# Kernel tuning notes

Measured on AMD Instinct MI355X. Metric: run time of the kernel, lower is better.

## Reference

```python
import jax, jax.numpy as jnp
import numpy as np

NUM_HEADS = 16
KEY_DIM = 64
B, S, D = 2, 2048, 1024


def setup_inputs() -> dict:
    key = jax.random.key(0)
    ks = jax.random.split(key, 5)
    scale = 1.0 / np.sqrt(D)
    return {
        "x": jax.random.normal(ks[0], (B, S, D), dtype=jnp.float32),
        "Wq": jax.random.normal(ks[1], (D, NUM_HEADS * KEY_DIM), dtype=jnp.float32) * scale,
        "Wk": jax.random.normal(ks[2], (D, NUM_HEADS * KEY_DIM), dtype=jnp.float32) * scale,
        "Wv": jax.random.normal(ks[3], (D, NUM_HEADS * KEY_DIM), dtype=jnp.float32) * scale,
        "Wo": jax.random.normal(ks[4], (NUM_HEADS * KEY_DIM, D), dtype=jnp.float32) * scale,
    }


def reference(x, Wq, Wk, Wv, Wo):
    b, s, d = x.shape
    h, kd = NUM_HEADS, KEY_DIM
    # QKV projections -> [B, H, S, Kd]
    q = (x @ Wq).reshape(b, s, h, kd).transpose(0, 2, 1, 3)
    k = (x @ Wk).reshape(b, s, h, kd).transpose(0, 2, 1, 3)
    v = (x @ Wv).reshape(b, s, h, kd).transpose(0, 2, 1, 3)
    # scaled dot-product attention, full [B,H,S,S] scores (faithful to source)
    logits = jnp.einsum("bhqd,bhkd->bhqk", q, k) / jnp.sqrt(jnp.float32(kd))
    attn = jax.nn.softmax(logits, axis=-1)
    out = jnp.einsum("bhqk,bhkd->bhqd", attn, v)  # [B,H,S,Kd]
    out = out.transpose(0, 2, 1, 3).reshape(b, s, h * kd)
    return out @ Wo
```

## Files before the change

### kernel.cpp

```cpp
#include <hip/hip_runtime.h>


typedef __attribute__((ext_vector_type(8))) short short8;
typedef __attribute__((ext_vector_type(4))) float f32x4;

#define M_ROWS 4096
#define N_COLS 1024
#define K_DIM  1024
#define SEQ    2048

#define QSCALE 0.18033688011111772f

#if defined(__has_builtin)
#if __has_builtin(__builtin_amdgcn_exp2f)
#define EXP2(x) __builtin_amdgcn_exp2f(x)
#endif
#endif
#ifndef EXP2
#define EXP2(x) exp2f(x)
#endif

#define WAITCNT_VM8 0x0F78
#define WAITCNT_VM4 0x0F74

__device__ inline unsigned short f2bf(float f) {
  unsigned int u = __float_as_uint(f);
  u += 0x7fffu + ((u >> 16) & 1u);
  return (unsigned short)(u >> 16);
}

__device__ inline unsigned int pack2bf(float a, float b) {
  unsigned int ua = __float_as_uint(a); ua += 0x7fffu + ((ua >> 16) & 1u);
  unsigned int ub = __float_as_uint(b); ub += 0x7fffu + ((ub >> 16) & 1u);
  return (ua >> 16) | (ub & 0xffff0000u);
}

__device__ inline unsigned int cvtpk(float lo, float hi) {
  unsigned int r;
  asm("v_cvt_pk_bf16_f32 %0, %1, %2" : "=v"(r) : "v"(lo), "v"(hi));
  return r;
}

__device__ inline void swap32(unsigned int& a, unsigned int& b) {
  asm volatile("v_permlane32_swap_b32 %0, %1" : "+v"(a), "+v"(b));
}
__device__ inline void swap16(unsigned int& a, unsigned int& b) {
  asm volatile("v_permlane16_swap_b32 %0, %1" : "+v"(a), "+v"(b));
}

__device__ inline void async_load16(const unsigned short* gptr, unsigned short* lptr) {
  __builtin_amdgcn_global_load_lds(
      (const __attribute__((address_space(1))) unsigned int*)gptr,
      (__attribute__((address_space(3))) unsigned int*)lptr, 16, 0, 0);
}

__global__ void detect_kernel(const unsigned short* __restrict__ x, int* __restrict__ flag) {
  __shared__ int bad;
  if (threadIdx.x == 0) bad = 0;
  __syncthreads();
  for (int i = threadIdx.x; i < 1024; i += 256) {
    float f = __uint_as_float((unsigned int)x[i] << 16);
    float a = fabsf(f);
    if (!(a < 1e4f)) atomicOr(&bad, 1);
  }
  __syncthreads();
  if (threadIdx.x == 0) *flag = bad ? 0 : 1;
}

__global__ void convert_kernel(const void* __restrict__ src, unsigned short* __restrict__ dst,
                               int n4, const int* __restrict__ flag) {
  const int isbf = *flag;
  const int stride = gridDim.x * blockDim.x;
  for (int i = blockIdx.x * blockDim.x + threadIdx.x; i < n4; i += stride) {
    if (isbf) {
      ((uint2*)dst)[i] = ((const uint2*)src)[i];
    } else {
      float4 v = ((const float4*)src)[i];
      ushort4 o;
      o.x = f2bf(v.x); o.y = f2bf(v.y); o.z = f2bf(v.z); o.w = f2bf(v.w);
      ((ushort4*)dst)[i] = o;
    }
  }
}

__global__ __launch_bounds__(256) void convert_wT4_kernel(
    const void* __restrict__ s0, const void* __restrict__ s1,
    const void* __restrict__ s2, const void* __restrict__ s3,
    unsigned short* __restrict__ d0, unsigned short* __restrict__ d1,
    unsigned short* __restrict__ d2, unsigned short* __restrict__ d3,
    const int* __restrict__ flag) {
  __shared__ unsigned short t[32][33];
  const int z = blockIdx.z;
  const void* src = (z == 0) ? s0 : (z == 1) ? s1 : (z == 2) ? s2 : s3;
  unsigned short* dst = (z == 0) ? d0 : (z == 1) ? d1 : (z == 2) ? d2 : d3;
  const int tid = threadIdx.x;
  const int r0 = blockIdx.y * 32, c0 = blockIdx.x * 32;
  const int kr = tid >> 3, nc = (tid & 7) * 4;
  if (*flag) {
    const unsigned short* W = (const unsigned short*)src;
    uint2 v = *(const uint2*)(W + (size_t)(r0 + kr) * K_DIM + c0 + nc);
    t[kr][nc] = v.x & 0xffff; t[kr][nc + 1] = v.x >> 16;
    t[kr][nc + 2] = v.y & 0xffff; t[kr][nc + 3] = v.y >> 16;
  } else {
    const float* W = (const float*)src;
    float4 v = *(const float4*)(W + (size_t)(r0 + kr) * K_DIM + c0 + nc);
    t[kr][nc] = f2bf(v.x); t[kr][nc + 1] = f2bf(v.y);
    t[kr][nc + 2] = f2bf(v.z); t[kr][nc + 3] = f2bf(v.w);
  }
  __syncthreads();
  const int nr = tid >> 3, kc = (tid & 7) * 4;
  uint2 w;
  w.x = (unsigned int)t[kc][nr] | ((unsigned int)t[kc + 1][nr] << 16);
  w.y = (unsigned int)t[kc + 2][nr] | ((unsigned int)t[kc + 3][nr] << 16);
  *(uint2*)(dst + (size_t)(c0 + nr) * K_DIM + r0 + kc) = w;
}

#define GEMM_DMA(Aptr, Bptr, KTOT, KB, BUF)                                       \
  _Pragma("unroll") for (int r = 0; r < 2; ++r) {                                 \
    int s = r * 256 + wave * 64 + lane;                                           \
    int row = s >> 2, c = s & 3;                                                  \
    int g = c ^ ((row ^ (row >> 2)) & 3);                                         \
    async_load16((Aptr) + (size_t)(m0 + row) * (KTOT) + (KB) + g * 8,             \
                 &As[BUF][(size_t)(r * 256 + wave * 64) * 8]);                    \
    async_load16((Bptr) + (size_t)(n0 + row) * (KTOT) + (KB) + g * 8,             \
                 &Bs[BUF][(size_t)(r * 256 + wave * 64) * 8]);                    \
  }

#define GEMM_MAIN_LOOP(Aptr, Bptr, KTOT)                                          \
  f32x4 acc[4][4];                                                                \
  _Pragma("unroll") for (int i = 0; i < 4; ++i)                                   \
  _Pragma("unroll") for (int j = 0; j < 4; ++j)                                   \
      acc[i][j] = (f32x4){0.f, 0.f, 0.f, 0.f};                                    \
  const int xr = (l15 ^ (l15 >> 2)) & 3;                                          \
  GEMM_DMA(Aptr, Bptr, KTOT, 0, 0)                                                \
  for (int kb = 0; kb < (KTOT); kb += 32) {                                       \
    const int pp = (kb >> 5) & 1;                                                 \
    const int kbn = (kb + 32) & ((KTOT) - 1);                                     \
    GEMM_DMA(Aptr, Bptr, KTOT, kbn, pp ^ 1)                                       \
    __builtin_amdgcn_s_waitcnt(WAITCNT_VM4);                                      \
    __syncthreads();                                                              \
    short8 am[4], bn[4];                                                          \
    _Pragma("unroll") for (int i = 0; i < 4; ++i) {                               \
      int arow = wr * 64 + i * 16 + l15;                                          \
      int brow = wc * 64 + i * 16 + l15;                                          \
      int cc = quad ^ xr;                                                         \
      am[i] = *(const short8*)(&As[pp][arow * 32 + cc * 8]);                      \
      bn[i] = *(const short8*)(&Bs[pp][brow * 32 + cc * 8]);                      \
    }                                                                             \
    _Pragma("unroll") for (int i = 0; i < 4; ++i)                                 \
    _Pragma("unroll") for (int j = 0; j < 4; ++j)                                 \
        acc[i][j] = __builtin_amdgcn_mfma_f32_16x16x32_bf16(am[i], bn[j],         \
                                                            acc[i][j], 0, 0, 0); \
    __syncthreads();                                                              \
  }

__global__ __launch_bounds__(256, 3) void qkv_gemm_kernel(
    const unsigned short* __restrict__ Xb,
    const unsigned short* __restrict__ Wqt,
    const unsigned short* __restrict__ Wkt,
    const unsigned short* __restrict__ Wvt,
    unsigned short* __restrict__ Qb,
    unsigned short* __restrict__ Kb,
    unsigned short* __restrict__ Vt) {
  __shared__ __align__(16) unsigned short As[2][128 * 32];
  __shared__ __align__(16) unsigned short Bs[2][128 * 32];
  const int tid = threadIdx.x;
  const int wave = tid >> 6, lane = tid & 63;
  const int quad = lane >> 4, l15 = lane & 15;
  const int wr = wave >> 1, wc = wave & 1;
  const int m0 = blockIdx.x * 128;
  const int n0 = blockIdx.y * 128;
  const int wsel = blockIdx.z;
  const unsigned short* __restrict__ Bt =
      (wsel == 0) ? Wqt : ((wsel == 1) ? Wkt : Wvt);

  GEMM_MAIN_LOOP(Xb, Bt, K_DIM)

#pragma unroll
  for (int i = 0; i < 4; ++i) {
#pragma unroll
    for (int j = 0; j < 4; ++j) {
      int mbase = m0 + wr * 64 + i * 16 + quad * 4;
      int n = n0 + wc * 64 + j * 16 + l15;
      int h = n >> 6, d = n & 63;
      if (wsel == 2) {
        int b_ = mbase >> 11, s = mbase & 2047;
        uint2 w;
        w.x = cvtpk(acc[i][j][0], acc[i][j][1]);
        w.y = cvtpk(acc[i][j][2], acc[i][j][3]);
        *(uint2*)(Vt + ((size_t)(b_ * 16 + h) * 64 + d) * SEQ + s) = w;
      } else {
#pragma unroll
        for (int r = 0; r < 4; ++r) {
          int m = mbase + r;
          int b_ = m >> 11, s = m & 2047;
          float val = acc[i][j][r];
          if (wsel == 0)
            Qb[((size_t)(b_ * 16 + h) * SEQ + s) * 64 + d] = f2bf(val * QSCALE);
          else
            Kb[((size_t)(b_ * 16 + h) * SEQ + s) * 64 + d] = f2bf(val);
        }
      }
    }
  }
}

__global__ __launch_bounds__(256, 2) void flash_kernel(
    const unsigned short* __restrict__ Qb,
    const unsigned short* __restrict__ Kb,
    const unsigned short* __restrict__ Vt,
    unsigned short* __restrict__ Ob) {
  __shared__ __align__(16) unsigned short Klds[2][128 * 64];
  __shared__ __align__(16) unsigned short Vlds[2][64 * 128];
  const int tid = threadIdx.x;
  const int wave = tid >> 6, lane = tid & 63;
  const int quad = lane >> 4, l15 = lane & 15;
  const int bh = blockIdx.y;
  const int qbase = blockIdx.x * 128 + wave * 32;

  const unsigned short* __restrict__ Qp = Qb + (size_t)bh * SEQ * 64;
  const unsigned short* __restrict__ Kp = Kb + (size_t)bh * SEQ * 64;
  const unsigned short* __restrict__ Vp = Vt + (size_t)bh * 64 * SEQ;

  short8 qf[2][2];
#pragma unroll
  for (int g = 0; g < 2; ++g)
#pragma unroll
    for (int h = 0; h < 2; ++h)
      qf[g][h] = *(const short8*)(Qp + (size_t)(qbase + g * 16 + l15) * 64 + h * 32 + quad * 8);

  f32x4 O[2][4];
#pragma unroll
  for (int g = 0; g < 2; ++g)
#pragma unroll
    for (int t = 0; t < 4; ++t) O[g][t] = (f32x4){0.f, 0.f, 0.f, 0.f};
  float l_i[2] = {0.f, 0.f};

#define FLASH_DMA(KB, BUF)                                                     \
  _Pragma("unroll") for (int r = 0; r < 4; ++r) {                              \
    int s = r * 256 + tid;                                                     \
    int krow = s >> 3, kc = s & 7;                                             \
    int kg = kc ^ (krow & 7);                                                  \
    async_load16(Kp + (size_t)((KB) + krow) * 64 + kg * 8,                     \
                 &Klds[BUF][(size_t)(r * 256 + wave * 64) * 8]);               \
    int vrow = s >> 4, vc = s & 15;                                            \
    int vg = vc ^ (vrow & 15);                                                 \
    async_load16(Vp + (size_t)vrow * SEQ + (KB) + vg * 8,                      \
                 &Vlds[BUF][(size_t)(r * 256 + wave * 64) * 8]);               \
  }

  FLASH_DMA(0, 0)

  for (int kb = 0; kb < SEQ; kb += 128) {
    const int p = (kb >> 7) & 1;
    const int kbn = (kb + 128) & (SEQ - 1);
    FLASH_DMA(kbn, p ^ 1)
    __builtin_amdgcn_s_waitcnt(WAITCNT_VM8);
    __syncthreads();

    f32x4 sT[2][8];
    __builtin_amdgcn_s_setprio(1);
#pragma unroll
    for (int t = 0; t < 8; ++t) {
      int row = t * 16 + l15;
      int c0 = quad ^ (row & 7), c1 = (quad + 4) ^ (row & 7);
      short8 k0 = *(const short8*)(&Klds[p][row * 64 + c0 * 8]);
      short8 k1 = *(const short8*)(&Klds[p][row * 64 + c1 * 8]);
      sT[0][t] = __builtin_amdgcn_mfma_f32_16x16x32_bf16(k0, qf[0][0],
                 (f32x4){0.f, 0.f, 0.f, 0.f}, 0, 0, 0);
      sT[0][t] = __builtin_amdgcn_mfma_f32_16x16x32_bf16(k1, qf[0][1], sT[0][t], 0, 0, 0);
      sT[1][t] = __builtin_amdgcn_mfma_f32_16x16x32_bf16(k0, qf[1][0],
                 (f32x4){0.f, 0.f, 0.f, 0.f}, 0, 0, 0);
      sT[1][t] = __builtin_amdgcn_mfma_f32_16x16x32_bf16(k1, qf[1][1], sT[1][t], 0, 0, 0);
    }
    __builtin_amdgcn_s_setprio(0);

    short8 pb[2][4];
#pragma unroll
    for (int g = 0; g < 2; ++g) {
      float rs = 0.f;
      unsigned int wx[8], wy[8];
#pragma unroll
      for (int t = 0; t < 8; ++t) {
        float p0 = EXP2(sT[g][t][0]);
        float p1 = EXP2(sT[g][t][1]);
        float p2 = EXP2(sT[g][t][2]);
        float p3 = EXP2(sT[g][t][3]);
        rs += (p0 + p1) + (p2 + p3);
        wx[t] = cvtpk(p0, p1);
        wy[t] = cvtpk(p2, p3);
      }
      rs += __shfl_xor(rs, 16);
      rs += __shfl_xor(rs, 32);
      l_i[g] += rs;

#pragma unroll
      for (int m = 0; m < 4; ++m) {
        unsigned int a = wx[2 * m], c = wx[2 * m + 1];
        unsigned int b = wy[2 * m], d = wy[2 * m + 1];
        swap32(a, c); swap16(a, c);
        swap32(b, d); swap16(b, d);
        union { short8 s; unsigned int u[4]; } P;
        P.u[0] = a; P.u[1] = b; P.u[2] = c; P.u[3] = d;
        pb[g][m] = P.s;
      }
    }

    __builtin_amdgcn_s_setprio(1);
#pragma unroll
    for (int td = 0; td < 4; ++td) {
      int row = td * 16 + l15;
#pragma unroll
      for (int m = 0; m < 4; ++m) {
        short8 vf = *(const short8*)(&Vlds[p][row * 128 + (((m * 4 + quad) ^ l15) * 8)]);
        O[0][td] = __builtin_amdgcn_mfma_f32_16x16x32_bf16(vf, pb[0][m], O[0][td], 0, 0, 0);
        O[1][td] = __builtin_amdgcn_mfma_f32_16x16x32_bf16(vf, pb[1][m], O[1][td], 0, 0, 0);
      }
    }
    __builtin_amdgcn_s_setprio(0);
    __syncthreads();
  }

  const int b_ = bh >> 4, h = bh & 15;
#pragma unroll
  for (int g = 0; g < 2; ++g) {
    const float inv = 1.f / l_i[g];
    unsigned short* orow = Ob + ((size_t)(b_ * SEQ) + qbase + g * 16 + l15) * N_COLS + h * 64;
#pragma unroll
    for (int t = 0; t < 4; ++t) {
      uint2 w;
      w.x = cvtpk(O[g][t][0] * inv, O[g][t][1] * inv);
      w.y = cvtpk(O[g][t][2] * inv, O[g][t][3] * inv);
      *(uint2*)(orow + t * 16 + quad * 4) = w;
    }
  }
#undef FLASH_DMA
}

__global__ __launch_bounds__(256, 3) void out_gemm_kernel(
    const unsigned short* __restrict__ Ob,
    const unsigned short* __restrict__ Wot,
    void* __restrict__ out,
    const int* __restrict__ flag) {
  __shared__ __align__(16) unsigned short As[2][128 * 32];
  __shared__ __align__(16) unsigned short Bs[2][128 * 32];
  const int tid = threadIdx.x;
  const int wave = tid >> 6, lane = tid & 63;
  const int quad = lane >> 4, l15 = lane & 15;
  const int wr = wave >> 1, wc = wave & 1;
  const int m0 = blockIdx.x * 128;
  const int n0 = blockIdx.y * 128;
  const int isbf = *flag;

  GEMM_MAIN_LOOP(Ob, Wot, N_COLS)

#pragma unroll
  for (int i = 0; i < 4; ++i) {
#pragma unroll
    for (int j = 0; j < 4; ++j) {
      int mbase = m0 + wr * 64 + i * 16 + quad * 4;
      int n = n0 + wc * 64 + j * 16 + l15;
#pragma unroll
      for (int r = 0; r < 4; ++r) {
        float val = acc[i][j][r];
        if (isbf) ((unsigned short*)out)[(size_t)(mbase + r) * K_DIM + n] = f2bf(val);
        else      ((float*)out)[(size_t)(mbase + r) * K_DIM + n] = val;
      }
    }
  }
}

extern "C" void kernel_launch(void* const* d_in, const int* in_sizes, int n_in,
                              void* d_out, int out_size, void* d_ws, size_t ws_size,
                              hipStream_t stream) {
  const void* x  = d_in[0];
  const void* wq = d_in[1];
  const void* wk = d_in[2];
  const void* wv = d_in[3];
  const void* wo = d_in[4];

  char* ws = (char*)d_ws;
  size_t off = 0;
  int* flag = (int*)(ws + off);                 off += 256;
  unsigned short* xb  = (unsigned short*)(ws + off); off += (size_t)M_ROWS * K_DIM * 2;
  unsigned short* wqt = (unsigned short*)(ws + off); off += (size_t)K_DIM * N_COLS * 2;
  unsigned short* wkt = (unsigned short*)(ws + off); off += (size_t)K_DIM * N_COLS * 2;
  unsigned short* wvt = (unsigned short*)(ws + off); off += (size_t)K_DIM * N_COLS * 2;
  unsigned short* wot = (unsigned short*)(ws + off); off += (size_t)N_COLS * K_DIM * 2;
  unsigned short* Qb  = (unsigned short*)(ws + off); off += (size_t)M_ROWS * 1024 * 2;
  unsigned short* Kb  = (unsigned short*)(ws + off); off += (size_t)M_ROWS * 1024 * 2;
  unsigned short* Vtb = (unsigned short*)(ws + off); off += (size_t)M_ROWS * 1024 * 2;
  unsigned short* Ob  = (unsigned short*)(ws + off); off += (size_t)M_ROWS * N_COLS * 2;
  (void)ws_size; (void)in_sizes; (void)n_in; (void)out_size;

  detect_kernel<<<1, 256, 0, stream>>>((const unsigned short*)x, flag);

  convert_kernel<<<2048, 256, 0, stream>>>(x, xb, (M_ROWS * K_DIM) / 4, flag);
  convert_wT4_kernel<<<dim3(32, 32, 4), 256, 0, stream>>>(wq, wk, wv, wo,
                                                          wqt, wkt, wvt, wot, flag);

  qkv_gemm_kernel<<<dim3(32, 8, 3), 256, 0, stream>>>(xb, wqt, wkt, wvt, Qb, Kb, Vtb);
  flash_kernel<<<dim3(16, 32), 256, 0, stream>>>(Qb, Kb, Vtb, Ob);
  out_gemm_kernel<<<dim3(32, 8), 256, 0, stream>>>(Ob, wot, d_out, flag);
}
```

Baseline: 190.2 us.

## Shrink flash attention tiles to 64 queries and 64-key blocks for occupancy

Each flash block now handles 64 query rows (16 per wave instead of 32) and steps through keys in 64-wide chunks. LDS per block is halved, launch bounds rise to 4 blocks per CU, and the grid doubles to 1024 blocks. The goal is better occupancy and latency hiding. The cost is that each K/V tile is reused by half as many queries, which doubles K/V traffic and adds more barrier iterations.

```diff
diff --git a/kernel.cpp b/kernel.cpp
--- a/kernel.cpp
+++ b/kernel.cpp
@@ -205,105 +205,93 @@
   }
 }
 
-__global__ __launch_bounds__(256, 2) void flash_kernel(
+__global__ __launch_bounds__(256, 4) void flash_kernel(
     const unsigned short* __restrict__ Qb,
     const unsigned short* __restrict__ Kb,
     const unsigned short* __restrict__ Vt,
     unsigned short* __restrict__ Ob) {
-  __shared__ __align__(16) unsigned short Klds[2][128 * 64];
-  __shared__ __align__(16) unsigned short Vlds[2][64 * 128];
+  __shared__ __align__(16) unsigned short Klds[2][64 * 64];
+  __shared__ __align__(16) unsigned short Vlds[2][64 * 64];
   const int tid = threadIdx.x;
   const int wave = tid >> 6, lane = tid & 63;
   const int quad = lane >> 4, l15 = lane & 15;
   const int bh = blockIdx.y;
-  const int qbase = blockIdx.x * 128 + wave * 32;
+  const int qbase = blockIdx.x * 64 + wave * 16;
 
   const unsigned short* __restrict__ Qp = Qb + (size_t)bh * SEQ * 64;
   const unsigned short* __restrict__ Kp = Kb + (size_t)bh * SEQ * 64;
   const unsigned short* __restrict__ Vp = Vt + (size_t)bh * 64 * SEQ;
 
-  short8 qf[2][2];
-#pragma unroll
-  for (int g = 0; g < 2; ++g)
-#pragma unroll
-    for (int h = 0; h < 2; ++h)
-      qf[g][h] = *(const short8*)(Qp + (size_t)(qbase + g * 16 + l15) * 64 + h * 32 + quad * 8);
-
-  f32x4 O[2][4];
-#pragma unroll
-  for (int g = 0; g < 2; ++g)
-#pragma unroll
-    for (int t = 0; t < 4; ++t) O[g][t] = (f32x4){0.f, 0.f, 0.f, 0.f};
-  float l_i[2] = {0.f, 0.f};
+  short8 qf[2];
+#pragma unroll
+  for (int h = 0; h < 2; ++h)
+    qf[h] = *(const short8*)(Qp + (size_t)(qbase + l15) * 64 + h * 32 + quad * 8);
+
+  f32x4 O[4];
+#pragma unroll
+  for (int t = 0; t < 4; ++t) O[t] = (f32x4){0.f, 0.f, 0.f, 0.f};
+  float l_i = 0.f;
 
 #define FLASH_DMA(KB, BUF)                                                     \
-  _Pragma("unroll") for (int r = 0; r < 4; ++r) {                              \
+  _Pragma("unroll") for (int r = 0; r < 2; ++r) {                              \
     int s = r * 256 + tid;                                                     \
-    int krow = s >> 3, kc = s & 7;                                             \
-    int kg = kc ^ (krow & 7);                                                  \
-    async_load16(Kp + (size_t)((KB) + krow) * 64 + kg * 8,                     \
+    int row = s >> 3, c = s & 7;                                               \
+    int g = c ^ (row & 7);                                                     \
+    async_load16(Kp + (size_t)((KB) + row) * 64 + g * 8,                       \
                  &Klds[BUF][(size_t)(r * 256 + wave * 64) * 8]);               \
-    int vrow = s >> 4, vc = s & 15;                                            \
-    int vg = vc ^ (vrow & 15);                                                 \
-    async_load16(Vp + (size_t)vrow * SEQ + (KB) + vg * 8,                      \
+    async_load16(Vp + (size_t)row * SEQ + (KB) + g * 8,                        \
                  &Vlds[BUF][(size_t)(r * 256 + wave * 64) * 8]);               \
   }
 
   FLASH_DMA(0, 0)
 
-  for (int kb = 0; kb < SEQ; kb += 128) {
-    const int p = (kb >> 7) & 1;
-    const int kbn = (kb + 128) & (SEQ - 1);
+  for (int kb = 0; kb < SEQ; kb += 64) {
+    const int p = (kb >> 6) & 1;
+    const int kbn = (kb + 64) & (SEQ - 1);
     FLASH_DMA(kbn, p ^ 1)
-    __builtin_amdgcn_s_waitcnt(WAITCNT_VM8);
+    __builtin_amdgcn_s_waitcnt(WAITCNT_VM4);
     __syncthreads();
 
-    f32x4 sT[2][8];
+    f32x4 sT[4];
     __builtin_amdgcn_s_setprio(1);
 #pragma unroll
-    for (int t = 0; t < 8; ++t) {
+    for (int t = 0; t < 4; ++t) {
       int row = t * 16 + l15;
       int c0 = quad ^ (row & 7), c1 = (quad + 4) ^ (row & 7);
       short8 k0 = *(const short8*)(&Klds[p][row * 64 + c0 * 8]);
       short8 k1 = *(const short8*)(&Klds[p][row * 64 + c1 * 8]);
-      sT[0][t] = __builtin_amdgcn_mfma_f32_16x16x32_bf16(k0, qf[0][0],
-                 (f32x4){0.f, 0.f, 0.f, 0.f}, 0, 0, 0);
-      sT[0][t] = __builtin_amdgcn_mfma_f32_16x16x32_bf16(k1, qf[0][1], sT[0][t], 0, 0, 0);
-      sT[1][t] = __builtin_amdgcn_mfma_f32_16x16x32_bf16(k0, qf[1][0],
-                 (f32x4){0.f, 0.f, 0.f, 0.f}, 0, 0, 0);
-      sT[1][t] = __builtin_amdgcn_mfma_f32_16x16x32_bf16(k1, qf[1][1], sT[1][t], 0, 0, 0);
+      sT[t] = __builtin_amdgcn_mfma_f32_16x16x32_bf16(k0, qf[0],
+              (f32x4){0.f, 0.f, 0.f, 0.f}, 0, 0, 0);
+      sT[t] = __builtin_amdgcn_mfma_f32_16x16x32_bf16(k1, qf[1], sT[t], 0, 0, 0);
     }
     __builtin_amdgcn_s_setprio(0);
 
-    short8 pb[2][4];
-#pragma unroll
-    for (int g = 0; g < 2; ++g) {
-      float rs = 0.f;
-      unsigned int wx[8], wy[8];
-#pragma unroll
-      for (int t = 0; t < 8; ++t) {
-        float p0 = EXP2(sT[g][t][0]);
-        float p1 = EXP2(sT[g][t][1]);
-        float p2 = EXP2(sT[g][t][2]);
-        float p3 = EXP2(sT[g][t][3]);
-        rs += (p0 + p1) + (p2 + p3);
-        wx[t] = cvtpk(p0, p1);
-        wy[t] = cvtpk(p2, p3);
-      }
-      rs += __shfl_xor(rs, 16);
-      rs += __shfl_xor(rs, 32);
-      l_i[g] += rs;
-
-#pragma unroll
-      for (int m = 0; m < 4; ++m) {
-        unsigned int a = wx[2 * m], c = wx[2 * m + 1];
-        unsigned int b = wy[2 * m], d = wy[2 * m + 1];
-        swap32(a, c); swap16(a, c);
-        swap32(b, d); swap16(b, d);
-        union { short8 s; unsigned int u[4]; } P;
-        P.u[0] = a; P.u[1] = b; P.u[2] = c; P.u[3] = d;
-        pb[g][m] = P.s;
-      }
+    float rs = 0.f;
+    unsigned int wx[4], wy[4];
+#pragma unroll
+    for (int t = 0; t < 4; ++t) {
+      float p0 = EXP2(sT[t][0]);
+      float p1 = EXP2(sT[t][1]);
+      float p2 = EXP2(sT[t][2]);
+      float p3 = EXP2(sT[t][3]);
+      rs += (p0 + p1) + (p2 + p3);
+      wx[t] = cvtpk(p0, p1);
+      wy[t] = cvtpk(p2, p3);
+    }
+    rs += __shfl_xor(rs, 16);
+    rs += __shfl_xor(rs, 32);
+    l_i += rs;
+
+    short8 pb[2];
+#pragma unroll
+    for (int m = 0; m < 2; ++m) {
+      unsigned int a = wx[2 * m], c = wx[2 * m + 1];
+      unsigned int b = wy[2 * m], d = wy[2 * m + 1];
+      swap32(a, c); swap16(a, c);
+      swap32(b, d); swap16(b, d);
+      union { short8 s; unsigned int u[4]; } P;
+      P.u[0] = a; P.u[1] = b; P.u[2] = c; P.u[3] = d;
+      pb[m] = P.s;
     }
 
     __builtin_amdgcn_s_setprio(1);
@@ -311,10 +299,9 @@
     for (int td = 0; td < 4; ++td) {
       int row = td * 16 + l15;
 #pragma unroll
-      for (int m = 0; m < 4; ++m) {
-        short8 vf = *(const short8*)(&Vlds[p][row * 128 + (((m * 4 + quad) ^ l15) * 8)]);
-        O[0][td] = __builtin_amdgcn_mfma_f32_16x16x32_bf16(vf, pb[0][m], O[0][td], 0, 0, 0);
-        O[1][td] = __builtin_amdgcn_mfma_f32_16x16x32_bf16(vf, pb[1][m], O[1][td], 0, 0, 0);
+      for (int m = 0; m < 2; ++m) {
+        short8 vf = *(const short8*)(&Vlds[p][row * 64 + (((m * 4 + quad) ^ (row & 7)) * 8)]);
+        O[td] = __builtin_amdgcn_mfma_f32_16x16x32_bf16(vf, pb[m], O[td], 0, 0, 0);
       }
     }
     __builtin_amdgcn_s_setprio(0);
@@ -322,17 +309,14 @@
   }
 
   const int b_ = bh >> 4, h = bh & 15;
-#pragma unroll
-  for (int g = 0; g < 2; ++g) {
-    const float inv = 1.f / l_i[g];
-    unsigned short* orow = Ob + ((size_t)(b_ * SEQ) + qbase + g * 16 + l15) * N_COLS + h * 64;
-#pragma unroll
-    for (int t = 0; t < 4; ++t) {
-      uint2 w;
-      w.x = cvtpk(O[g][t][0] * inv, O[g][t][1] * inv);
-      w.y = cvtpk(O[g][t][2] * inv, O[g][t][3] * inv);
-      *(uint2*)(orow + t * 16 + quad * 4) = w;
-    }
+  const float inv = 1.f / l_i;
+  unsigned short* orow = Ob + ((size_t)(b_ * SEQ) + qbase + l15) * N_COLS + h * 64;
+#pragma unroll
+  for (int t = 0; t < 4; ++t) {
+    uint2 w;
+    w.x = cvtpk(O[t][0] * inv, O[t][1] * inv);
+    w.y = cvtpk(O[t][2] * inv, O[t][3] * inv);
+    *(uint2*)(orow + t * 16 + quad * 4) = w;
   }
 #undef FLASH_DMA
 }
@@ -400,6 +384,6 @@
                                                           wqt, wkt, wvt, wot, flag);
 
   qkv_gemm_kernel<<<dim3(32, 8, 3), 256, 0, stream>>>(xb, wqt, wkt, wvt, Qb, Kb, Vtb);
-  flash_kernel<<<dim3(16, 32), 256, 0, stream>>>(Qb, Kb, Vtb, Ob);
+  flash_kernel<<<dim3(32, 32), 256, 0, stream>>>(Qb, Kb, Vtb, Ob);
   out_gemm_kernel<<<dim3(32, 8), 256, 0, stream>>>(Ob, wot, d_out, flag);
 }
```

After: 196.7 us. 3.4% more time.
